# Performance work log

Measured on AMD Instinct MI355X. Metric: run time of the kernel, lower is better.

## Reference

```python
import jax, jax.numpy as jnp
import numpy as np

N_FFT = 512
HOP = 128
SR = 16000
N_MELS = N_FFT // 2 + 1  # 257, per __init__ (n_mels = n_fft//2+1)
EPS, S, ALPHA, DELTA, R = 1e-6, 0.025, 0.98, 2.0, 0.5  # pcenfunc defaults


def _mel_fbanks():
    # torchaudio melscale_fbanks with mel_scale='htk', norm=None, f_min=0, f_max=sr/2
    n_freqs = N_FFT // 2 + 1
    all_freqs = np.linspace(0.0, SR / 2.0, n_freqs)
    hz2mel = lambda f: 2595.0 * np.log10(1.0 + f / 700.0)
    mel2hz = lambda m: 700.0 * (10.0 ** (m / 2595.0) - 1.0)
    m_pts = np.linspace(hz2mel(0.0), hz2mel(SR / 2.0), N_MELS + 2)
    f_pts = mel2hz(m_pts)
    f_diff = f_pts[1:] - f_pts[:-1]
    slopes = f_pts[None, :] - all_freqs[:, None]  # (n_freqs, n_mels+2)
    down = -slopes[:, :-2] / f_diff[:-1]
    up = slopes[:, 2:] / f_diff[1:]
    fb = np.maximum(0.0, np.minimum(down, up))  # (n_freqs, n_mels)
    return jnp.asarray(fb, jnp.float32)


def _stft(sig, window):
    # torch.stft: center=True, reflect pad, win_length=n_fft, onesided
    pad = N_FFT // 2
    xp = jnp.pad(sig, (pad, pad), mode='reflect')
    n_frames = 1 + (xp.shape[0] - N_FFT) // HOP
    idx = jnp.arange(n_frames)[:, None] * HOP + jnp.arange(N_FFT)[None, :]
    frames = xp[idx] * window  # (frames, n_fft)
    return jnp.fft.rfft(frames, axis=-1)  # (frames, freq)


def _unwrap_time(p):
    # np.unwrap along the frames axis (axis=0 here since layout is (frames, freq))
    dd = jnp.diff(p, axis=0)
    ddmod = jnp.mod(dd + jnp.pi, 2.0 * jnp.pi) - jnp.pi
    ddmod = jnp.where((ddmod == -jnp.pi) & (dd > 0), jnp.pi, ddmod)
    corr = jnp.where(jnp.abs(dd) < jnp.pi, 0.0, ddmod - dd)
    return p + jnp.pad(jnp.cumsum(corr, axis=0), ((1, 0), (0, 0)))


def _pcen(x):
    # x: (frames, n_mels); m_0 = s*x_0, m_t = (1-s)*m_{t-1} + s*x_t
    m0 = S * x[0]
    def step(m, xt):
        m = (1.0 - S) * m + S * xt
        return m, m
    _, ms = jax.lax.scan(step, m0, x[1:])
    M = jnp.concatenate([m0[None], ms], axis=0)
    return (x / (M + EPS) ** ALPHA + DELTA) ** R - DELTA ** R


def setup_inputs() -> dict:
    key = jax.random.key(0)
    T = 4_800_000  # 5 minutes @ 16 kHz -> frames = 37501
    audio = jax.random.normal(key, (1, T), dtype=jnp.float32)
    return {"audio": audio, "mel_fbanks": _mel_fbanks()}


def reference(audio, mel_fbanks):
    sig = audio[0]  # batch of 1, as in the original (squeeze/unsqueeze)
    # torch.stft with window=None uses a rectangular (ones) window
    spec = _stft(sig, jnp.ones((N_FFT,), jnp.float32))  # (frames, freq) complex
    log_mag = jnp.log(jnp.abs(spec) + 1e-9)  # (frames, freq)
    # demodulated phase (on-device unwrap replaces the CPU round-trip)
    phase = _unwrap_time(jnp.angle(spec))
    real_demod = jnp.sin(phase)
    imag_demod = jnp.cos(phase)
    # MelSpectrogram: hann (periodic) window, power=2
    n = jnp.arange(N_FFT)
    hann = (0.5 * (1.0 - jnp.cos(2.0 * jnp.pi * n / N_FFT))).astype(jnp.float32)
    mspec = jnp.abs(_stft(sig, hann)) ** 2  # (frames, freq)
    mel = mspec @ mel_fbanks  # (frames, n_mels)
    pcen = _pcen(mel)  # (frames, n_mels); n_mels == freq here
    # perm(2,0,1) on (1, freq, frames) then cat along dim 1 -> (frames, 4, freq)
    data = jnp.stack([log_mag, pcen, real_demod, imag_demod], axis=1)
    # F.normalize(data, dim=0): L2 over the frames axis, eps=1e-12
    norm = jnp.maximum(jnp.linalg.norm(data, axis=0, keepdims=True), 1e-12)
    return data / norm
```

## Files before the change

kernel.cpp:

```cpp
#include <hip/hip_runtime.h>
#include <math.h>

#define NFFT 512
#define HOP 128
#define NBINS 257
#define ROW 1028
#define CHUNK 64
#define LAM64 0.19783147f
#define NG1F 512
#define NG1C 128
#define SWZ(a) ((a) ^ (((a) >> 4) & 15))

__device__ __forceinline__ float2 cmul(float2 a, float2 b) {
  return make_float2(a.x * b.x - a.y * b.y, a.x * b.y + a.y * b.x);
}

struct EB { float lg, sv, cv, msp; };

__global__ void k_prep(const float* __restrict__ fb, int* __restrict__ lohi,
                       float2* __restrict__ twg) {
  int t = threadIdx.x;
  for (int i = t; i < NFFT; i += 256) {
    double ang = -6.283185307179586476925286766559 * (double)i / (double)NFFT;
    twg[i] = make_float2((float)cos(ang), (float)sin(ang));
  }
  for (int m = t; m < NBINS; m += 256) {
    int lo = 0, hi = -1;
    for (int f = 0; f < NBINS; ++f) {
      if (fb[f * NBINS + m] != 0.0f) { if (hi < 0) lo = f; hi = f; }
    }
    lohi[m] = lo;
    lohi[NBINS + m] = hi;
  }
}

__device__ __forceinline__ EB epilogue_bin(const float2* __restrict__ S, int off,
                                           float* __restrict__ out, unsigned ob,
                                           int k, bool store) {
  float2 z = S[SWZ(off + k)];
  float mag, sv, cv;
  if (k == 0 || k == 256) {
    mag = fabsf(z.x);
    sv = (z.x < 0.0f) ? -8.742278e-8f : 0.0f;
    cv = copysignf(1.0f, z.x);
  } else {
    float r2 = fmaf(z.x, z.x, z.y * z.y);
    if (r2 > 0.0f) {
      float rs = __builtin_amdgcn_rsqf(r2);
      mag = r2 * rs;
      sv = z.y * rs;
      cv = z.x * rs;
    } else { mag = 0.0f; sv = 0.0f; cv = 1.0f; }
  }
  float lg = __logf(mag + 1e-9f);
  if (store) {
    out[ob + k] = lg;
    out[ob + 2 * NBINS + k] = sv;
    out[ob + 3 * NBINS + k] = cv;
  }
  float2 zm, zp;
  if (k == 0) { float2 s1 = S[SWZ(off + 1)]; zm = make_float2(s1.x, -s1.y); }
  else zm = S[SWZ(off + k - 1)];
  zp = S[SWZ(off + k + 1)];
  float hr = 0.5f * z.x - 0.25f * (zm.x + zp.x);
  float hi = 0.5f * z.y - 0.25f * (zm.y + zp.y);
  EB e; e.lg = lg; e.sv = sv; e.cv = cv; e.msp = hr * hr + hi * hi;
  return e;
}

__device__ __forceinline__ void unpack_bin(const float2* __restrict__ x,
                                           float2* __restrict__ y, int k) {
  float2 Zk, Zm;
  if (k <= 255) {
    float2 a0 = x[SWZ(k)], a1 = x[SWZ(k + 256)];
    Zk = make_float2(a0.x + a1.x, a0.y + a1.y);
  } else {
    float2 a0 = x[SWZ(k - 256)], a1 = x[SWZ(k)];
    Zk = make_float2(a0.x - a1.x, a0.y - a1.y);
  }
  int m2 = (NFFT - k) & (NFFT - 1);
  if (k == 0 || k == 256) {
    Zm = Zk;
  } else if (m2 >= 256) {
    float2 b0 = x[SWZ(m2 - 256)], b1 = x[SWZ(m2)];
    Zm = make_float2(b0.x - b1.x, b0.y - b1.y);
  } else {
    float2 b0 = x[SWZ(m2)], b1 = x[SWZ(m2 + 256)];
    Zm = make_float2(b0.x + b1.x, b0.y + b1.y);
  }
  y[SWZ(k)] = make_float2(0.5f * (Zk.x + Zm.x), 0.5f * (Zk.y - Zm.y));
  y[SWZ(258 + k)] = make_float2(0.5f * (Zk.y + Zm.y), 0.5f * (Zm.x - Zk.x));
}

__global__ __launch_bounds__(256) void k_fft(
    const float* __restrict__ audio, const float* __restrict__ fb,
    const int* __restrict__ lohi, const float2* __restrict__ twg,
    float* __restrict__ out, float* __restrict__ partF, int T, int nframes) {
  __shared__ float2 bufA[2][520];
  __shared__ float2 bufB[2][520];

  const int t = threadIdx.x;
  const int ff = t >> 7;
  const int v = t & 127;
  const int frb = blockIdx.x * 4;
  const int fr0 = frb + 2 * ff;
  const int fr1 = fr0 + 1;
  const bool h0 = fr0 < nframes;
  const bool h1 = fr1 < nframes;

  float2* __restrict__ xa = bufA[ff];
  float2* __restrict__ xb = bufB[ff];

  float2 wreg[4][3];
  {
    const int qms[4] = {v, v & ~3, v & ~15, v & ~63};
#pragma unroll
    for (int s = 0; s < 4; ++s) {
      wreg[s][0] = twg[qms[s]];
      wreg[s][1] = twg[2 * qms[s]];
      wreg[s][2] = twg[3 * qms[s]];
    }
  }

  int s0 = fr0 * HOP - NFFT / 2;
  float2 xr[4];
#pragma unroll
  for (int j = 0; j < 4; ++j) {
    int i = v + 128 * j;
    int q0 = s0 + i;
    if (q0 < 0) q0 = -q0;
    if (q0 >= T) q0 = 2 * T - 2 - q0;
    int q1 = s0 + HOP + i;
    if (q1 < 0) q1 = -q1;
    if (q1 >= T) q1 = 2 * T - 2 - q1;
    xr[j] = make_float2(audio[q0], h1 ? audio[q1] : 0.0f);
  }
  {
    float2 s02 = make_float2(xr[0].x + xr[2].x, xr[0].y + xr[2].y);
    float2 d02 = make_float2(xr[0].x - xr[2].x, xr[0].y - xr[2].y);
    float2 s13 = make_float2(xr[1].x + xr[3].x, xr[1].y + xr[3].y);
    float2 d13 = make_float2(xr[1].x - xr[3].x, xr[1].y - xr[3].y);
    int o = 4 * v;
    xb[SWZ(o)] = make_float2(s02.x + s13.x, s02.y + s13.y);
    xb[SWZ(o + 1)] = cmul(wreg[0][0], make_float2(d02.x + d13.y, d02.y - d13.x));
    xb[SWZ(o + 2)] = cmul(wreg[0][1], make_float2(s02.x - s13.x, s02.y - s13.y));
    xb[SWZ(o + 3)] = cmul(wreg[0][2], make_float2(d02.x - d13.y, d02.y + d13.x));
  }
  __syncthreads();

  const int ra0 = SWZ(v), ra1 = SWZ(v + 128), ra2 = SWZ(v + 256), ra3 = SWZ(v + 384);
  float2* x = xb;
  float2* y = xa;
#pragma unroll
  for (int ds = 1; ds < 4; ++ds) {
    const int m = 1 << (2 * ds);
    int qm = v & ~(m - 1);
    int r = v - qm;
    int o = 4 * qm + r;
    float2 x0 = x[ra0], x1 = x[ra1], x2 = x[ra2], x3 = x[ra3];
    float2 s02 = make_float2(x0.x + x2.x, x0.y + x2.y);
    float2 d02 = make_float2(x0.x - x2.x, x0.y - x2.y);
    float2 s13 = make_float2(x1.x + x3.x, x1.y + x3.y);
    float2 d13 = make_float2(x1.x - x3.x, x1.y - x3.y);
    float2 E0 = make_float2(s02.x + s13.x, s02.y + s13.y);
    float2 u1 = make_float2(d02.x + d13.y, d02.y - d13.x);
    float2 u2 = make_float2(s02.x - s13.x, s02.y - s13.y);
    float2 u3 = make_float2(d02.x - d13.y, d02.y + d13.x);
    float2 E1 = cmul(wreg[ds][0], u1);
    float2 E2 = cmul(wreg[ds][1], u2);
    float2 E3 = cmul(wreg[ds][2], u3);
    y[SWZ(o)] = E0;
    y[SWZ(o + m)] = E1;
    y[SWZ(o + 2 * m)] = E2;
    y[SWZ(o + 3 * m)] = E3;
    __syncthreads();
    float2* tmp = x; x = y; y = tmp;
  }
  unpack_bin(x, y, v);
  unpack_bin(x, y, v + 128);
  if (v < 2) unpack_bin(x, y, 256 + v);
  __syncthreads();

  unsigned ob0 = (unsigned)fr0 * ROW;
  unsigned ob1 = (unsigned)fr1 * ROW;
  float mspA[2], mspB[2], sql[2], sqs[2], sqc[2];
#pragma unroll
  for (int ki = 0; ki < 2; ++ki) {
    int k = v + 128 * ki;
    EB e0 = epilogue_bin(y, 0, out, ob0, k, h0);
    EB e1 = epilogue_bin(y, 258, out, ob1, k, h1);
    mspA[ki] = e0.msp;
    mspB[ki] = e1.msp;
    sql[ki] = (h0 ? e0.lg * e0.lg : 0.f) + (h1 ? e1.lg * e1.lg : 0.f);
    sqs[ki] = (h0 ? e0.sv * e0.sv : 0.f) + (h1 ? e1.sv * e1.sv : 0.f);
    sqc[ki] = (h0 ? e0.cv * e0.cv : 0.f) + (h1 ? e1.cv * e1.cv : 0.f);
  }
  float mspA6 = 0.f, mspB6 = 0.f, sql6 = 0.f, sqs6 = 0.f, sqc6 = 0.f;
  if (v == 0) {
    EB e0 = epilogue_bin(y, 0, out, ob0, 256, h0);
    EB e1 = epilogue_bin(y, 258, out, ob1, 256, h1);
    mspA6 = e0.msp;
    mspB6 = e1.msp;
    sql6 = (h0 ? e0.lg * e0.lg : 0.f) + (h1 ? e1.lg * e1.lg : 0.f);
    sqs6 = (h0 ? e0.sv * e0.sv : 0.f) + (h1 ? e1.sv * e1.sv : 0.f);
    sqc6 = (h0 ? e0.cv * e0.cv : 0.f) + (h1 ? e1.cv * e1.cv : 0.f);
  }
  __syncthreads();

  float* mspSh = (float*)&bufB[ff][0];
  float* sqf = (float*)&bufA[ff][0];
#pragma unroll
  for (int ki = 0; ki < 2; ++ki) {
    int k = v + 128 * ki;
    mspSh[k] = mspA[ki];
    mspSh[258 + k] = mspB[ki];
    sqf[k] = sql[ki];
    sqf[258 + k] = sqs[ki];
    sqf[516 + k] = sqc[ki];
  }
  if (v == 0) {
    mspSh[256] = mspA6;
    mspSh[258 + 256] = mspB6;
    sqf[256] = sql6;
    sqf[258 + 256] = sqs6;
    sqf[516 + 256] = sqc6;
  }
  __syncthreads();

  for (int m = v; m < NBINS; m += 128) {
    int lo = lohi[m], hi = lohi[NBINS + m];
    float a0 = 0.0f, a1 = 0.0f;
    for (int f = lo; f <= hi; ++f) {
      float w = fb[f * NBINS + m];
      a0 = fmaf(mspSh[f], w, a0);
      a1 = fmaf(mspSh[258 + f], w, a1);
    }
    if (h0) out[ob0 + NBINS + m] = a0;
    if (h1) out[ob1 + NBINS + m] = a1;
  }

  const float* sq0 = (const float*)&bufA[0][0];
  const float* sq1 = (const float*)&bufA[1][0];
  for (int i = t; i < 771; i += 256) {
    int lidx = i + (i >= 257) + (i >= 514);
    partF[(unsigned)blockIdx.x * 771u + i] = sq0[lidx] + sq1[lidx];
  }
}

__global__ __launch_bounds__(320) void k_pcen_a(const float* __restrict__ out,
                                                float* __restrict__ mend, int nframes) {
  int m = threadIdx.x;
  if (m >= NBINS) return;
  int c = blockIdx.x;
  int F0 = c * CHUNK;
  int end = min(F0 + CHUNK, nframes);
  const float SS = 0.025f, OMS = 1.0f - SS;
  float mm = 0.0f;
  int tf = F0;
  for (; tf + 16 <= end; tf += 16) {
    float xs[16];
#pragma unroll
    for (int j = 0; j < 16; ++j) xs[j] = out[(unsigned)(tf + j) * ROW + NBINS + m];
#pragma unroll
    for (int j = 0; j < 16; ++j) mm = OMS * mm + SS * xs[j];
  }
  for (; tf < end; ++tf) mm = OMS * mm + SS * out[(unsigned)tf * ROW + NBINS + m];
  mend[c * NBINS + m] = mm;
}

__global__ __launch_bounds__(320) void k_pcen_c(float* __restrict__ out,
                                                const float* __restrict__ mend,
                                                float* __restrict__ partC,
                                                int nframes) {
  int m = threadIdx.x;
  if (m >= NBINS) return;
  int c = blockIdx.x;
  int F0 = c * CHUNK;
  int end = min(F0 + CHUNK, nframes);
  const float SS = 0.025f, OMS = 1.0f - SS;
  const float SQ2 = sqrtf(2.0f);
  float mm;
  if (c >= 12) {
    float xs[12];
#pragma unroll
    for (int j = 0; j < 12; ++j) xs[j] = mend[(c - 12 + j) * NBINS + m];
    mm = 0.0f;
#pragma unroll
    for (int j = 0; j < 12; ++j) mm = xs[j] + LAM64 * mm;
  } else {
    mm = 0.0f;
    for (int j = 0; j < c; ++j) mm = mend[j * NBINS + m] + LAM64 * mm;
  }
  float acc1 = 0.0f;
  int tf = F0;
  for (; tf + 16 <= end; tf += 16) {
    float xs[16], ys[16];
#pragma unroll
    for (int j = 0; j < 16; ++j) xs[j] = out[(unsigned)(tf + j) * ROW + NBINS + m];
#pragma unroll
    for (int j = 0; j < 16; ++j) {
      mm = OMS * mm + SS * xs[j];
      float invden = __expf(-0.98f * __logf(mm + 1e-6f));
      float val = fmaf(xs[j], invden, 2.0f);
      float rs = __builtin_amdgcn_rsqf(val);
      ys[j] = val * rs - SQ2;
      acc1 = fmaf(ys[j], ys[j], acc1);
    }
#pragma unroll
    for (int j = 0; j < 16; ++j) out[(unsigned)(tf + j) * ROW + NBINS + m] = ys[j];
  }
  for (; tf < end; ++tf) {
    unsigned idx = (unsigned)tf * ROW + NBINS + m;
    float xv = out[idx];
    mm = OMS * mm + SS * xv;
    float invden = __expf(-0.98f * __logf(mm + 1e-6f));
    float val = fmaf(xv, invden, 2.0f);
    float rs = __builtin_amdgcn_rsqf(val);
    float yv = val * rs - SQ2;
    acc1 = fmaf(yv, yv, acc1);
    out[idx] = yv;
  }
  partC[c * NBINS + m] = acc1;
}

__global__ __launch_bounds__(256) void k_norm1(const float* __restrict__ partF,
                                               const float* __restrict__ partC,
                                               float* __restrict__ part2F,
                                               float* __restrict__ part2C,
                                               int nfb, int chunks) {
  int t = threadIdx.x;
  int b = blockIdx.x;
  if (b < NG1F) {
    int per = (nfb + NG1F - 1) / NG1F;
    int r0 = b * per, r1 = min(r0 + per, nfb);
    float a0 = 0.f, a1 = 0.f, a2 = 0.f, a3 = 0.f;
    int r = r0;
    for (; r + 4 <= r1; r += 4) {
      float x0[4], x1[4], x2[4], x3[4];
#pragma unroll
      for (int j = 0; j < 4; ++j) {
        unsigned base = (unsigned)(r + j) * 771u;
        x0[j] = partF[base + t];
        x1[j] = partF[base + t + 256];
        x2[j] = (t + 512 < 771) ? partF[base + t + 512] : 0.f;
        x3[j] = (t < 3) ? partF[base + t + 768] : 0.f;
      }
#pragma unroll
      for (int j = 0; j < 4; ++j) {
        a0 += x0[j]; a1 += x1[j]; a2 += x2[j]; a3 += x3[j];
      }
    }
    for (; r < r1; ++r) {
      unsigned base = (unsigned)r * 771u;
      a0 += partF[base + t];
      a1 += partF[base + t + 256];
      if (t + 512 < 771) a2 += partF[base + t + 512];
      if (t < 3) a3 += partF[base + t + 768];
    }
    part2F[(unsigned)t * NG1F + b] = a0;
    part2F[(unsigned)(t + 256) * NG1F + b] = a1;
    if (t + 512 < 771) part2F[(unsigned)(t + 512) * NG1F + b] = a2;
    if (t < 3) part2F[(unsigned)(t + 768) * NG1F + b] = a3;
  } else {
    int rg = b - NG1F;
    int per = (chunks + NG1C - 1) / NG1C;
    int r0 = rg * per, r1 = min(r0 + per, chunks);
    float a0 = 0.f, a1 = 0.f;
    int r = r0;
    for (; r + 4 <= r1; r += 4) {
      float x0[4], x1[4];
#pragma unroll
      for (int j = 0; j < 4; ++j) {
        unsigned base = (unsigned)(r + j) * 257u;
        x0[j] = partC[base + t];
        x1[j] = (t == 0) ? partC[base + 256] : 0.f;
      }
#pragma unroll
      for (int j = 0; j < 4; ++j) { a0 += x0[j]; a1 += x1[j]; }
    }
    for (; r < r1; ++r) {
      unsigned base = (unsigned)r * 257u;
      a0 += partC[base + t];
      if (t == 0) a1 += partC[base + 256];
    }
    part2C[(unsigned)t * NG1C + rg] = a0;
    if (t == 0) part2C[256u * NG1C + rg] = a1;
  }
}

__global__ __launch_bounds__(256) void k_norm2(const float* __restrict__ part2F,
                                               const float* __restrict__ part2C,
                                               float* __restrict__ invn) {
  __shared__ float red[256];
  int c = blockIdx.x, t = threadIdx.x;
  float s;
  if (c >= 257 && c < 514) {
    int m = c - 257;
    s = (t < NG1C) ? part2C[(unsigned)m * NG1C + t] : 0.f;
  } else {
    int i = (c < 257) ? c : c - 257;
    s = part2F[(unsigned)i * NG1F + t] + part2F[(unsigned)i * NG1F + t + 256];
  }
  red[t] = s;
  __syncthreads();
  for (int o = 128; o > 0; o >>= 1) {
    if (t < o) red[t] += red[t + o];
    __syncthreads();
  }
  if (t == 0) invn[c] = 1.0f / fmaxf(sqrtf(red[0]), 1e-12f);
}

__global__ __launch_bounds__(320) void k_scale(float4* __restrict__ out4,
                                               const float* __restrict__ invn,
                                               int nframes) {
  int t = threadIdx.x;
  if (t >= 257) return;
  float4 iv = make_float4(invn[4 * t], invn[4 * t + 1], invn[4 * t + 2], invn[4 * t + 3]);
  for (unsigned fr = blockIdx.x; fr < (unsigned)nframes; fr += gridDim.x) {
    unsigned idx = fr * 257u + t;
    float4 v = out4[idx];
    v.x *= iv.x;
    v.y *= iv.y;
    v.z *= iv.z;
    v.w *= iv.w;
    out4[idx] = v;
  }
}

extern "C" void kernel_launch(void* const* d_in, const int* in_sizes, int n_in,
                              void* d_out, int out_size, void* d_ws, size_t ws_size,
                              hipStream_t stream) {
  const float* audio = (const float*)d_in[0];
  const float* fb = (const float*)d_in[1];
  int T = in_sizes[0];
  int nframes = 1 + T / HOP;
  float* out = (float*)d_out;
  int chunks = (nframes + CHUNK - 1) / CHUNK;
  int nfb = (nframes + 3) / 4;

  float* wsf = (float*)d_ws;
  float2* twg = (float2*)wsf;
  float* mend = wsf + 1024;
  float* invn = mend + (long)chunks * NBINS;
  int* lohi = (int*)(invn + ROW);
  float* partC = (float*)(lohi + 2 * NBINS);
  float* part2F = partC + (long)chunks * NBINS;
  float* part2C = part2F + 771L * NG1F;
  float* partF = part2C + 257L * NG1C;

  k_prep<<<1, 256, 0, stream>>>(fb, lohi, twg);
  k_fft<<<nfb, 256, 0, stream>>>(audio, fb, lohi, twg, out, partF, T, nframes);
  k_pcen_a<<<chunks, 320, 0, stream>>>(out, mend, nframes);
  k_pcen_c<<<chunks, 320, 0, stream>>>(out, mend, partC, nframes);
  k_norm1<<<NG1F + NG1C, 256, 0, stream>>>(partF, partC, part2F, part2C, nfb, chunks);
  k_norm2<<<ROW, 256, 0, stream>>>(part2F, part2C, invn);
  k_scale<<<2048, 320, 0, stream>>>((float4*)out, invn, nframes);
}
```

Baseline: 187.6 us.

## Fuse PCEN segment partial sums into FFT kernel and load twiddles per stage

The FFT kernel now also computes, for each block of four frames, the EMA contribution of those frames to the PCEN state and writes it to a small segment buffer. The first PCEN pass then combines 16 segment values per chunk with a fixed decay factor, so it no longer re-reads all mel outputs from global memory. Twiddle factors are now loaded inside each radix-4 stage instead of being preloaded into a 12-entry register array, which lowers register pressure at the cost of more global or cache loads. An extra barrier and extra LDS traffic are added to the FFT kernel, and the segment arithmetic relies on the hard-coded decay constants being correct.

```diff
diff --git a/kernel.cpp b/kernel.cpp
--- a/kernel.cpp
+++ b/kernel.cpp
@@ -7,6 +7,7 @@
 #define ROW 1028
 #define CHUNK 64
 #define LAM64 0.19783147f
+#define LAM4  0.90368789f
 #define NG1F 512
 #define NG1C 128
 #define SWZ(a) ((a) ^ (((a) >> 4) & 15))
@@ -95,7 +96,8 @@
 __global__ __launch_bounds__(256) void k_fft(
     const float* __restrict__ audio, const float* __restrict__ fb,
     const int* __restrict__ lohi, const float2* __restrict__ twg,
-    float* __restrict__ out, float* __restrict__ partF, int T, int nframes) {
+    float* __restrict__ out, float* __restrict__ partF,
+    float* __restrict__ segB, int T, int nframes) {
   __shared__ float2 bufA[2][520];
   __shared__ float2 bufB[2][520];
 
@@ -110,17 +112,6 @@
 
   float2* __restrict__ xa = bufA[ff];
   float2* __restrict__ xb = bufB[ff];
-
-  float2 wreg[4][3];
-  {
-    const int qms[4] = {v, v & ~3, v & ~15, v & ~63};
-#pragma unroll
-    for (int s = 0; s < 4; ++s) {
-      wreg[s][0] = twg[qms[s]];
-      wreg[s][1] = twg[2 * qms[s]];
-      wreg[s][2] = twg[3 * qms[s]];
-    }
-  }
 
   int s0 = fr0 * HOP - NFFT / 2;
   float2 xr[4];
@@ -136,15 +127,16 @@
     xr[j] = make_float2(audio[q0], h1 ? audio[q1] : 0.0f);
   }
   {
+    float2 w1 = twg[v], w2 = twg[2 * v], w3 = twg[3 * v];
     float2 s02 = make_float2(xr[0].x + xr[2].x, xr[0].y + xr[2].y);
     float2 d02 = make_float2(xr[0].x - xr[2].x, xr[0].y - xr[2].y);
     float2 s13 = make_float2(xr[1].x + xr[3].x, xr[1].y + xr[3].y);
     float2 d13 = make_float2(xr[1].x - xr[3].x, xr[1].y - xr[3].y);
     int o = 4 * v;
     xb[SWZ(o)] = make_float2(s02.x + s13.x, s02.y + s13.y);
-    xb[SWZ(o + 1)] = cmul(wreg[0][0], make_float2(d02.x + d13.y, d02.y - d13.x));
-    xb[SWZ(o + 2)] = cmul(wreg[0][1], make_float2(s02.x - s13.x, s02.y - s13.y));
-    xb[SWZ(o + 3)] = cmul(wreg[0][2], make_float2(d02.x - d13.y, d02.y + d13.x));
+    xb[SWZ(o + 1)] = cmul(w1, make_float2(d02.x + d13.y, d02.y - d13.x));
+    xb[SWZ(o + 2)] = cmul(w2, make_float2(s02.x - s13.x, s02.y - s13.y));
+    xb[SWZ(o + 3)] = cmul(w3, make_float2(d02.x - d13.y, d02.y + d13.x));
   }
   __syncthreads();
 
@@ -157,6 +149,9 @@
     int qm = v & ~(m - 1);
     int r = v - qm;
     int o = 4 * qm + r;
+    float2 w1 = twg[qm];
+    float2 w2 = twg[2 * qm];
+    float2 w3 = twg[3 * qm];
     float2 x0 = x[ra0], x1 = x[ra1], x2 = x[ra2], x3 = x[ra3];
     float2 s02 = make_float2(x0.x + x2.x, x0.y + x2.y);
     float2 d02 = make_float2(x0.x - x2.x, x0.y - x2.y);
@@ -166,9 +161,9 @@
     float2 u1 = make_float2(d02.x + d13.y, d02.y - d13.x);
     float2 u2 = make_float2(s02.x - s13.x, s02.y - s13.y);
     float2 u3 = make_float2(d02.x - d13.y, d02.y + d13.x);
-    float2 E1 = cmul(wreg[ds][0], u1);
-    float2 E2 = cmul(wreg[ds][1], u2);
-    float2 E3 = cmul(wreg[ds][2], u3);
+    float2 E1 = cmul(w1, u1);
+    float2 E2 = cmul(w2, u2);
+    float2 E3 = cmul(w3, u3);
     y[SWZ(o)] = E0;
     y[SWZ(o + m)] = E1;
     y[SWZ(o + 2 * m)] = E2;
@@ -237,34 +232,39 @@
     }
     if (h0) out[ob0 + NBINS + m] = a0;
     if (h1) out[ob1 + NBINS + m] = a1;
-  }
+    mspSh[520 + m] = fmaf(0.975f, a0, a1);
+  }
+  __syncthreads();
 
   const float* sq0 = (const float*)&bufA[0][0];
   const float* sq1 = (const float*)&bufA[1][0];
+  const float* pg0 = (const float*)&bufB[0][0];
+  const float* pg1 = (const float*)&bufB[1][0];
   for (int i = t; i < 771; i += 256) {
     int lidx = i + (i >= 257) + (i >= 514);
     partF[(unsigned)blockIdx.x * 771u + i] = sq0[lidx] + sq1[lidx];
   }
-}
-
-__global__ __launch_bounds__(320) void k_pcen_a(const float* __restrict__ out,
-                                                float* __restrict__ mend, int nframes) {
+  for (int i = t; i < NBINS; i += 256) {
+    segB[(unsigned)blockIdx.x * 257u + i] =
+        0.025f * fmaf(0.950625f, pg0[520 + i], pg1[520 + i]);
+  }
+}
+
+__global__ __launch_bounds__(320) void k_mend(const float* __restrict__ segB,
+                                              float* __restrict__ mend,
+                                              int nfb, int chunks) {
   int m = threadIdx.x;
   if (m >= NBINS) return;
   int c = blockIdx.x;
-  int F0 = c * CHUNK;
-  int end = min(F0 + CHUNK, nframes);
-  const float SS = 0.025f, OMS = 1.0f - SS;
+  float xs[16];
+#pragma unroll
+  for (int g = 0; g < 16; ++g) {
+    int b = 16 * c + g;
+    xs[g] = (b < nfb) ? segB[(unsigned)b * 257u + m] : 0.0f;
+  }
   float mm = 0.0f;
-  int tf = F0;
-  for (; tf + 16 <= end; tf += 16) {
-    float xs[16];
-#pragma unroll
-    for (int j = 0; j < 16; ++j) xs[j] = out[(unsigned)(tf + j) * ROW + NBINS + m];
-#pragma unroll
-    for (int j = 0; j < 16; ++j) mm = OMS * mm + SS * xs[j];
-  }
-  for (; tf < end; ++tf) mm = OMS * mm + SS * out[(unsigned)tf * ROW + NBINS + m];
+#pragma unroll
+  for (int g = 0; g < 16; ++g) mm = fmaf(LAM4, mm, xs[g]);
   mend[c * NBINS + m] = mm;
 }
 
@@ -446,11 +446,12 @@
   float* partC = (float*)(lohi + 2 * NBINS);
   float* part2F = partC + (long)chunks * NBINS;
   float* part2C = part2F + 771L * NG1F;
-  float* partF = part2C + 257L * NG1C;
+  float* segB = part2C + 257L * NG1C;
+  float* partF = segB + (long)nfb * NBINS;
 
   k_prep<<<1, 256, 0, stream>>>(fb, lohi, twg);
-  k_fft<<<nfb, 256, 0, stream>>>(audio, fb, lohi, twg, out, partF, T, nframes);
-  k_pcen_a<<<chunks, 320, 0, stream>>>(out, mend, nframes);
+  k_fft<<<nfb, 256, 0, stream>>>(audio, fb, lohi, twg, out, partF, segB, T, nframes);
+  k_mend<<<chunks, 320, 0, stream>>>(segB, mend, nfb, chunks);
   k_pcen_c<<<chunks, 320, 0, stream>>>(out, mend, partC, nframes);
   k_norm1<<<NG1F + NG1C, 256, 0, stream>>>(partF, partC, part2F, part2C, nfb, chunks);
   k_norm2<<<ROW, 256, 0, stream>>>(part2F, part2C, invn);
```

Measured after the change: 182.7 us, median of 2. 1.03x faster.
